# Optimization experiments

Hardware: AMD Instinct MI355X
Metric: run time of the kernel (lower is better)

The kernel has to match this reference:

```python
import jax, jax.numpy as jnp
import numpy as np

LN_EPS = 1e-5  # torch LayerNorm default
EPS = 1e-8     # slot-attention eps

def _ln(x, g, b):
    m = jnp.mean(x, axis=-1, keepdims=True)
    v = jnp.mean(jnp.square(x - m), axis=-1, keepdims=True)
    return (x - m) * jax.lax.rsqrt(v + LN_EPS) * g + b

def setup_inputs() -> dict:
    key = jax.random.key(0)
    ks = jax.random.split(key, 16)
    b, d, n_s, h = 131072, 256, 16, 256
    w_scale = d ** -0.5
    return {
        "inputs": jax.random.normal(ks[0], (b, 1, d), jnp.float32),
        "noise": jax.random.normal(ks[1], (n_s, d), jnp.float32),
        "slots_mu": jax.random.normal(ks[2], (1, d), jnp.float32),
        "slots_sigma": jax.random.uniform(ks[3], (1, d), jnp.float32),
        "Wq": jax.random.normal(ks[4], (d, d), jnp.float32) * w_scale,
        "bq": jnp.zeros((d,), jnp.float32),
        "Wk": jax.random.normal(ks[5], (d, d), jnp.float32) * w_scale,
        "bk": jnp.zeros((d,), jnp.float32),
        "Wv": jax.random.normal(ks[6], (d, d), jnp.float32) * w_scale,
        "bv": jnp.zeros((d,), jnp.float32),
        "W_ih": jax.random.normal(ks[7], (3 * d, d), jnp.float32) * w_scale,
        "W_hh": jax.random.normal(ks[8], (3 * d, d), jnp.float32) * w_scale,
        "b_ih": jnp.zeros((3 * d,), jnp.float32),
        "b_hh": jnp.zeros((3 * d,), jnp.float32),
        "W1": jax.random.normal(ks[9], (h, d), jnp.float32) * w_scale,
        "b1": jnp.zeros((h,), jnp.float32),
        "W2": jax.random.normal(ks[10], (d, h), jnp.float32) * (h ** -0.5),
        "b2": jnp.zeros((d,), jnp.float32),
        "g_in": jnp.ones((d,), jnp.float32),
        "be_in": jnp.zeros((d,), jnp.float32),
        "g_s": jnp.ones((d,), jnp.float32),
        "be_s": jnp.zeros((d,), jnp.float32),
        "g_f": jnp.ones((d,), jnp.float32),
        "be_f": jnp.zeros((d,), jnp.float32),
    }

def reference(inputs, noise, slots_mu, slots_sigma, Wq, bq, Wk, bk, Wv, bv,
              W_ih, W_hh, b_ih, b_hh, W1, b1, W2, b2,
              g_in, be_in, g_s, be_s, g_f, be_f):
    b, w, d = inputs.shape  # w == 1 required by the module's LayerNorm(dim)
    x = inputs.reshape(b, w * d)
    scale = d ** -0.5
    iters = 3

    slots = slots_mu + slots_sigma * noise  # (n_s, d), reparameterized normal

    x = _ln(x, g_in, be_in)
    k = x @ Wk.T + bk  # (b, d)
    v = x @ Wv.T + bv  # (b, d)

    for _ in range(iters):
        slots_prev = slots
        s = _ln(slots, g_s, be_s)
        q = s @ Wq.T + bq                      # (n_s, d)
        dots = jnp.einsum('nd,bd->nb', q, k) * scale
        attn = jax.nn.softmax(dots, axis=0) + EPS   # softmax over slots
        attn = attn / jnp.sum(attn, axis=-1, keepdims=True)
        updates = jnp.einsum('bd,nb->nd', v, attn)  # (n_s, d)
        # torch GRUCell
        gx = updates @ W_ih.T + b_ih                # (n_s, 3d)
        gh = slots_prev @ W_hh.T + b_hh
        xr, xz, xn = jnp.split(gx, 3, axis=-1)
        hr, hz, hn = jnp.split(gh, 3, axis=-1)
        r = jax.nn.sigmoid(xr + hr)
        z = jax.nn.sigmoid(xz + hz)
        n = jnp.tanh(xn + r * hn)
        slots = (1.0 - z) * n + z * slots_prev
        ff = jax.nn.relu(_ln(slots, g_f, be_f) @ W1.T + b1) @ W2.T + b2
        slots = slots + ff
    return slots
```

## Files before the change

### kernel.cpp

```cpp
#include <hip/hip_runtime.h>
#include <stdint.h>

#define B_ROWS 131072
#define SCALE 0.0625f
#define LN_EPS 1e-5f
#define ATTN_EPS 1e-8f

#define BIG_BLOCKS 512
#define BIG_THREADS 512
#define ROWS_PER_BLOCK (B_ROWS / BIG_BLOCKS)
#define ROWS_PER_WAVE  (ROWS_PER_BLOCK / 8)
#define NSLICE 64

#define WS_PARTU 0
#define WS_PARTS (WS_PARTU + 512*4096)
#define WS_U     (WS_PARTS + 512*16)
#define WS_S     (WS_U + 4096)
#define WS_SLOTS (WS_S + 64)
#define WS_MID   (WS_SLOTS + 4096)
#define WS_GX    (WS_MID + 4096)
#define WS_GH    (WS_GX + 12288)
#define WS_H1    (WS_GH + 12288)
#define WS_QKG   (WS_H1 + 4096)
#define WS_QB    (WS_QKG + 4096)
#define WS_WIHV  (WS_QB + 64)
#define WS_BGX   (WS_WIHV + 196608)
#define WS_WQKG  (WS_BGX + 768)
#define WS_U2G   (WS_WQKG + 65536)
#define WS_U1    (WS_U2G + 256)
#define WS_C1    (WS_U1 + 256)

__global__ __launch_bounds__(256) void k_pre1(
    const float* __restrict__ Wq, const float* __restrict__ bq,
    const float* __restrict__ Wk, const float* __restrict__ bk,
    const float* __restrict__ Wv, const float* __restrict__ bv,
    const float* __restrict__ W_ih, const float* __restrict__ b_ih,
    const float* __restrict__ g_in, const float* __restrict__ be_in,
    float* __restrict__ ws)
{
  int bid = blockIdx.x, t = threadIdx.x;
  int wave = t >> 6, lane = t & 63;
  if (bid < 256) {
#pragma unroll
    for (int q = 0; q < 4; q++)
      ws[WS_PARTU + bid * 1024 + q * 256 + t] = 0.f;
  } else {
#pragma unroll
    for (int q = 0; q < 4; q++)
      ws[WS_PARTS + q * 256 + t] = 0.f;
  }
  if (bid < 192) {
    __shared__ __align__(16) float sW[4 * 256];
    __shared__ __align__(16) float sBv[256];
    int j0 = bid * 4;
#pragma unroll
    for (int r = 0; r < 4; r++) sW[r * 256 + t] = W_ih[(j0 + r) * 256 + t];
    sBv[t] = bv[t];
    __syncthreads();
    int d = t;
    float a0 = 0.f, a1 = 0.f, a2 = 0.f, a3 = 0.f;
#pragma unroll 8
    for (int dd = 0; dd < 256; dd++) {
      float v = Wv[dd * 256 + d];
      a0 = fmaf(sW[0 * 256 + dd], v, a0);
      a1 = fmaf(sW[1 * 256 + dd], v, a1);
      a2 = fmaf(sW[2 * 256 + dd], v, a2);
      a3 = fmaf(sW[3 * 256 + dd], v, a3);
    }
    ws[WS_WIHV + (j0 + 0) * 256 + d] = a0;
    ws[WS_WIHV + (j0 + 1) * 256 + d] = a1;
    ws[WS_WIHV + (j0 + 2) * 256 + d] = a2;
    ws[WS_WIHV + (j0 + 3) * 256 + d] = a3;
    float s = 0.f;
#pragma unroll
    for (int q = 0; q < 4; q++) {
      int idx = lane * 4 + q;
      s = fmaf(sW[wave * 256 + idx], sBv[idx], s);
    }
#pragma unroll
    for (int m = 1; m <= 32; m <<= 1) s += __shfl_xor(s, m);
    if (lane == 0) ws[WS_BGX + j0 + wave] = b_ih[j0 + wave] + s;
  } else if (bid < 256) {
    __shared__ __align__(16) float sKc[4 * 256];
    __shared__ __align__(16) float sBq[256];
    int c0 = (bid - 192) * 4;
#pragma unroll
    for (int r = 0; r < 4; r++) sKc[r * 256 + t] = Wk[t * 256 + c0 + r];
    sBq[t] = bq[t];
    __syncthreads();
    int d = t;
    float a0 = 0.f, a1 = 0.f, a2 = 0.f, a3 = 0.f;
#pragma unroll 8
    for (int i = 0; i < 256; i++) {
      float wq = Wq[i * 256 + d];
      a0 = fmaf(wq, sKc[0 * 256 + i], a0);
      a1 = fmaf(wq, sKc[1 * 256 + i], a1);
      a2 = fmaf(wq, sKc[2 * 256 + i], a2);
      a3 = fmaf(wq, sKc[3 * 256 + i], a3);
    }
    ws[WS_WQKG + (c0 + 0) * 256 + d] = SCALE * g_in[c0 + 0] * a0;
    ws[WS_WQKG + (c0 + 1) * 256 + d] = SCALE * g_in[c0 + 1] * a1;
    ws[WS_WQKG + (c0 + 2) * 256 + d] = SCALE * g_in[c0 + 2] * a2;
    ws[WS_WQKG + (c0 + 3) * 256 + d] = SCALE * g_in[c0 + 3] * a3;
    float s = 0.f;
#pragma unroll
    for (int q = 0; q < 4; q++) {
      int idx = lane * 4 + q;
      s = fmaf(sBq[idx], sKc[wave * 256 + idx], s);
    }
#pragma unroll
    for (int m = 1; m <= 32; m <<= 1) s += __shfl_xor(s, m);
    if (lane == 0) ws[WS_U2G + c0 + wave] = SCALE * g_in[c0 + wave] * s;
  } else {
    __shared__ __align__(16) float sBe[256];
    __shared__ __align__(16) float sT2[256];
    sBe[t] = be_in[t];
    __syncthreads();
    float a = 0.f;
#pragma unroll 8
    for (int dp = 0; dp < 256; dp += 4) {
      float4 w = *(const float4*)(Wk + t * 256 + dp);
      a = fmaf(w.x, sBe[dp], fmaf(w.y, sBe[dp + 1],
          fmaf(w.z, sBe[dp + 2], fmaf(w.w, sBe[dp + 3], a))));
    }
    sT2[t] = a + bk[t];
    __syncthreads();
    float u = 0.f;
#pragma unroll 8
    for (int i = 0; i < 256; i++)
      u = fmaf(Wq[i * 256 + t], sT2[i], u);
    ws[WS_U1 + t] = u;
    if (wave == 0) {
      float s = 0.f;
#pragma unroll
      for (int q = 0; q < 4; q++) {
        int idx = lane * 4 + q;
        s = fmaf(bq[idx], sT2[idx], s);
      }
#pragma unroll
      for (int m = 1; m <= 32; m <<= 1) s += __shfl_xor(s, m);
      if (lane == 0) ws[WS_C1] = s;
    }
  }
}

__global__ __launch_bounds__(256) void k_qkg(
    const float* __restrict__ noise, const float* __restrict__ mu,
    const float* __restrict__ sigma, const float* __restrict__ g_s,
    const float* __restrict__ be_s, float* __restrict__ ws, int init)
{
  __shared__ __align__(16) float sS[16 * 260];
  __shared__ __align__(16) float sAux[512];
  __shared__ __align__(16) float sStat[32];
  int bid = blockIdx.x, t = threadIdx.x;
  for (int n = 0; n < 16; n++) {
    float v;
    if (init) v = fmaf(sigma[t], noise[n * 256 + t], mu[t]);
    else      v = ws[WS_SLOTS + n * 256 + t];
    sS[n * 260 + t] = v;
    if (init && bid == 0) ws[WS_SLOTS + n * 256 + t] = v;
  }
  __syncthreads();
  { int n = t >> 4, c = t & 15;
    float s1 = 0.f, s2 = 0.f;
    for (int k = 0; k < 16; k++) {
      float x = sS[n * 260 + c * 16 + k];
      s1 += x; s2 = fmaf(x, x, s2);
    }
    sAux[n * 16 + c] = s1; sAux[256 + n * 16 + c] = s2; }
  __syncthreads();
  if (t < 16) {
    float s1 = 0.f, s2 = 0.f;
    for (int c = 0; c < 16; c++) { s1 += sAux[t * 16 + c]; s2 += sAux[256 + t * 16 + c]; }
    float m = s1 * (1.f / 256.f);
    float v = fmaxf(fmaf(-m, m, s2 * (1.f / 256.f)), 0.f);
    sStat[t] = m; sStat[16 + t] = rsqrtf(v + LN_EPS);
  }
  __syncthreads();
  { float gs = g_s[t], bs = be_s[t];
    for (int n = 0; n < 16; n++) {
      float m = sStat[n], rs = sStat[16 + n];
      sS[n * 260 + t] = fmaf((sS[n * 260 + t] - m) * rs, gs, bs);
    } }
  __syncthreads();
  if (bid < 64) {
    int cr = t >> 6, n = (t >> 2) & 15, ks = t & 3;
    int c = bid * 4 + cr;
    const float* wrow = ws + WS_WQKG + c * 256 + ks * 64;
    const float* srow = &sS[n * 260 + ks * 64];
    float acc = 0.f;
#pragma unroll
    for (int i = 0; i < 16; i++) {
      float4 w = *(const float4*)(wrow + i * 4);
      float4 s4 = *(const float4*)(srow + i * 4);
      acc = fmaf(w.x, s4.x, fmaf(w.y, s4.y, fmaf(w.z, s4.z, fmaf(w.w, s4.w, acc))));
    }
    sAux[t] = acc;
    __syncthreads();
    if (t < 64) {
      int cr2 = t >> 4, n2 = t & 15;
      int c2 = bid * 4 + cr2;
      int b = cr2 * 64 + n2 * 4;
      float s = sAux[b] + sAux[b + 1] + sAux[b + 2] + sAux[b + 3];
      ws[WS_QKG + n2 * 256 + c2] = s + ws[WS_U2G + c2];
    }
  } else {
    int n = t >> 4, ks = t & 15;
    float acc = 0.f;
    for (int k = 0; k < 16; k++)
      acc = fmaf(sS[n * 260 + ks * 16 + k], ws[WS_U1 + ks * 16 + k], acc);
    sAux[t] = acc;
    __syncthreads();
    if (t < 16) {
      float s = 0.f;
      for (int k = 0; k < 16; k++) s += sAux[t * 16 + k];
      ws[WS_QB + t] = SCALE * (s + ws[WS_C1]);
    }
  }
}

__global__ __launch_bounds__(512, 2) void k_big(
    const float* __restrict__ X, float* __restrict__ ws)
{
  __shared__ __align__(16) float red[4 * 4096];
  __shared__ __align__(16) float redS[128];
  int t = threadIdx.x;
  int wave = t >> 6, lane = t & 63;
  int p = lane >> 4, g = lane & 15;

  const float* qkg = ws + WS_QKG;
  float qw[4][16];
  float qs[4];
#pragma unroll
  for (int i = 0; i < 4; i++) {
    const float* rp = qkg + (4 * p + i) * 256 + g * 16;
#pragma unroll
    for (int jq = 0; jq < 4; jq++) {
      float4 v4 = *(const float4*)(rp + 4 * jq);
      qw[i][4 * jq + 0] = v4.x; qw[i][4 * jq + 1] = v4.y;
      qw[i][4 * jq + 2] = v4.z; qw[i][4 * jq + 3] = v4.w;
    }
    float s = 0.f;
#pragma unroll
    for (int j = 0; j < 16; j++) s += qw[i][j];
    qs[i] = s;
  }
#pragma unroll
  for (int m = 1; m <= 8; m <<= 1) {
#pragma unroll
    for (int i = 0; i < 4; i++) qs[i] += __shfl_xor(qs[i], m);
  }
  float qb0[4];
  {
    float4 q4 = *(const float4*)(ws + WS_QB + 4 * p);
    qb0[0] = q4.x; qb0[1] = q4.y; qb0[2] = q4.z; qb0[3] = q4.w;
  }

  float P[4][16];
#pragma unroll
  for (int i = 0; i < 4; i++)
#pragma unroll
    for (int j = 0; j < 16; j++) P[i][j] = 0.f;
  float Q[4] = {0.f, 0.f, 0.f, 0.f};
  float Sa[4] = {0.f, 0.f, 0.f, 0.f};

  size_t rowbase = (size_t)blockIdx.x * ROWS_PER_BLOCK + (size_t)wave * ROWS_PER_WAVE;
  const float* base = X + rowbase * 256 + g * 16;

  float4 cA0 = *(const float4*)(base + 0);
  float4 cB0 = *(const float4*)(base + 4);
  float4 cC0 = *(const float4*)(base + 8);
  float4 cD0 = *(const float4*)(base + 12);
  float4 cA1 = *(const float4*)(base + 256);
  float4 cB1 = *(const float4*)(base + 260);
  float4 cC1 = *(const float4*)(base + 264);
  float4 cD1 = *(const float4*)(base + 268);

#pragma unroll 1
  for (int r = 0; r < ROWS_PER_WAVE; r += 2) {
    const float* nx = base + (size_t)((r + 2 < ROWS_PER_WAVE) ? (r + 2) : 0) * 256;
    float4 pA0 = *(const float4*)(nx + 0);
    float4 pB0 = *(const float4*)(nx + 4);
    float4 pC0 = *(const float4*)(nx + 8);
    float4 pD0 = *(const float4*)(nx + 12);
    float4 pA1 = *(const float4*)(nx + 256);
    float4 pB1 = *(const float4*)(nx + 260);
    float4 pC1 = *(const float4*)(nx + 264);
    float4 pD1 = *(const float4*)(nx + 268);

    float x0[16], x1[16];
    x0[0] = cA0.x; x0[1] = cA0.y; x0[2] = cA0.z; x0[3] = cA0.w;
    x0[4] = cB0.x; x0[5] = cB0.y; x0[6] = cB0.z; x0[7] = cB0.w;
    x0[8] = cC0.x; x0[9] = cC0.y; x0[10] = cC0.z; x0[11] = cC0.w;
    x0[12] = cD0.x; x0[13] = cD0.y; x0[14] = cD0.z; x0[15] = cD0.w;
    x1[0] = cA1.x; x1[1] = cA1.y; x1[2] = cA1.z; x1[3] = cA1.w;
    x1[4] = cB1.x; x1[5] = cB1.y; x1[6] = cB1.z; x1[7] = cB1.w;
    x1[8] = cC1.x; x1[9] = cC1.y; x1[10] = cC1.z; x1[11] = cC1.w;
    x1[12] = cD1.x; x1[13] = cD1.y; x1[14] = cD1.z; x1[15] = cD1.w;

    float s10 = 0.f, s20 = 0.f, s11 = 0.f, s21 = 0.f;
    float d0[4] = {0.f, 0.f, 0.f, 0.f};
    float d1[4] = {0.f, 0.f, 0.f, 0.f};
#pragma unroll
    for (int j = 0; j < 16; j++) {
      s10 += x0[j]; s20 = fmaf(x0[j], x0[j], s20);
      s11 += x1[j]; s21 = fmaf(x1[j], x1[j], s21);
#pragma unroll
      for (int i = 0; i < 4; i++) {
        d0[i] = fmaf(qw[i][j], x0[j], d0[i]);
        d1[i] = fmaf(qw[i][j], x1[j], d1[i]);
      }
    }
#pragma unroll
    for (int m = 1; m <= 8; m <<= 1) {
      s10 += __shfl_xor(s10, m); s11 += __shfl_xor(s11, m);
      s20 += __shfl_xor(s20, m); s21 += __shfl_xor(s21, m);
#pragma unroll
      for (int i = 0; i < 4; i++) {
        d0[i] += __shfl_xor(d0[i], m);
        d1[i] += __shfl_xor(d1[i], m);
      }
    }
    float mean0 = s10 * (1.f / 256.f), mean1 = s11 * (1.f / 256.f);
    float var0 = fmaxf(fmaf(-mean0, mean0, s20 * (1.f / 256.f)), 0.f);
    float var1 = fmaxf(fmaf(-mean1, mean1, s21 * (1.f / 256.f)), 0.f);
    float rs0 = rsqrtf(var0 + LN_EPS), rs1 = rsqrtf(var1 + LN_EPS);
    float mrs0 = mean0 * rs0, mrs1 = mean1 * rs1;

    float dsc0[4], dsc1[4];
#pragma unroll
    for (int i = 0; i < 4; i++) {
      dsc0[i] = fmaf(rs0, d0[i], fmaf(-mrs0, qs[i], qb0[i]));
      dsc1[i] = fmaf(rs1, d1[i], fmaf(-mrs1, qs[i], qb0[i]));
    }

    float mx0 = fmaxf(fmaxf(dsc0[0], dsc0[1]), fmaxf(dsc0[2], dsc0[3]));
    float mx1 = fmaxf(fmaxf(dsc1[0], dsc1[1]), fmaxf(dsc1[2], dsc1[3]));
    mx0 = fmaxf(mx0, __shfl_xor(mx0, 16)); mx1 = fmaxf(mx1, __shfl_xor(mx1, 16));
    mx0 = fmaxf(mx0, __shfl_xor(mx0, 32)); mx1 = fmaxf(mx1, __shfl_xor(mx1, 32));
    float e0[4], e1[4];
#pragma unroll
    for (int i = 0; i < 4; i++) {
      e0[i] = __expf(dsc0[i] - mx0);
      e1[i] = __expf(dsc1[i] - mx1);
    }
    float se0 = e0[0] + e0[1] + e0[2] + e0[3];
    float se1 = e1[0] + e1[1] + e1[2] + e1[3];
    se0 += __shfl_xor(se0, 16); se1 += __shfl_xor(se1, 16);
    se0 += __shfl_xor(se0, 32); se1 += __shfl_xor(se1, 32);
    float inv0 = 1.0f / se0, inv1 = 1.0f / se1;
    float a0v[4], ar0[4], a1v[4], ar1[4];
#pragma unroll
    for (int i = 0; i < 4; i++) {
      a0v[i] = fmaf(e0[i], inv0, ATTN_EPS); ar0[i] = a0v[i] * rs0;
      a1v[i] = fmaf(e1[i], inv1, ATTN_EPS); ar1[i] = a1v[i] * rs1;
    }

#pragma unroll
    for (int j = 0; j < 16; j++) {
#pragma unroll
      for (int i = 0; i < 4; i++) {
        P[i][j] = fmaf(ar0[i], x0[j], P[i][j]);
        P[i][j] = fmaf(ar1[i], x1[j], P[i][j]);
      }
    }
#pragma unroll
    for (int i = 0; i < 4; i++) {
      Q[i] = fmaf(a0v[i], mrs0, Q[i]);
      Q[i] = fmaf(a1v[i], mrs1, Q[i]);
      Sa[i] += a0v[i];
      Sa[i] += a1v[i];
    }

    cA0 = pA0; cB0 = pB0; cC0 = pC0; cD0 = pD0;
    cA1 = pA1; cB1 = pB1; cC1 = pC1; cD1 = pD1;
  }

  int slot = wave & 3;
  if (wave < 4) {
#pragma unroll
    for (int i = 0; i < 4; i++) {
#pragma unroll
      for (int jq = 0; jq < 4; jq++) {
        float4 v4;
        v4.x = P[i][4 * jq + 0] - Q[i]; v4.y = P[i][4 * jq + 1] - Q[i];
        v4.z = P[i][4 * jq + 2] - Q[i]; v4.w = P[i][4 * jq + 3] - Q[i];
        *(float4*)&red[slot * 4096 + (4 * p + i) * 256 + g * 16 + jq * 4] = v4;
      }
    }
  }
  if (g == 0) {
#pragma unroll
    for (int i = 0; i < 4; i++) redS[wave * 16 + 4 * p + i] = Sa[i];
  }
  __syncthreads();
  if (wave >= 4) {
#pragma unroll
    for (int i = 0; i < 4; i++) {
#pragma unroll
      for (int jq = 0; jq < 4; jq++) {
        float4* dst = (float4*)&red[slot * 4096 + (4 * p + i) * 256 + g * 16 + jq * 4];
        float4 c = *dst;
        c.x += P[i][4 * jq + 0] - Q[i]; c.y += P[i][4 * jq + 1] - Q[i];
        c.z += P[i][4 * jq + 2] - Q[i]; c.w += P[i][4 * jq + 3] - Q[i];
        *dst = c;
      }
    }
  }
  __syncthreads();
  int slice = blockIdx.x & 63;
#pragma unroll
  for (int k = 0; k < 8; k++) {
    int idx = k * 512 + t;
    float v = red[idx] + red[4096 + idx] + red[8192 + idx] + red[12288 + idx];
    atomicAdd(&ws[WS_PARTU + (size_t)slice * 4096 + idx], v);
  }
  if (t < 16) {
    float sv = 0.f;
#pragma unroll
    for (int w = 0; w < 8; w++) sv += redS[w * 16 + t];
    atomicAdd(&ws[WS_PARTS + slice * 16 + t], sv);
  }
}

__global__ __launch_bounds__(256) void k_red(float* __restrict__ ws)
{
  __shared__ __align__(16) float sAux[256];
  int bid = blockIdx.x, t = threadIdx.x;
  if (bid < 256) {
    int el = t & 15, wg = t >> 4;
    int e = bid * 16 + el;
    float acc = 0.f;
#pragma unroll
    for (int k = 0; k < 4; k++) {
      size_t idx = WS_PARTU + (size_t)(wg + k * 16) * 4096 + e;
      acc += ws[idx];
      ws[idx] = 0.f;
    }
    sAux[t] = acc;
    __syncthreads();
    if (t < 16) {
      float s = 0.f;
      for (int w = 0; w < 16; w++) s += sAux[w * 16 + t];
      ws[WS_U + bid * 16 + t] = s;
    }
  } else {
    int n = t & 15, wg = t >> 4;
    float acc = 0.f;
#pragma unroll
    for (int k = 0; k < 4; k++) {
      int idx = WS_PARTS + (wg + k * 16) * 16 + n;
      acc += ws[idx];
      ws[idx] = 0.f;
    }
    sAux[t] = acc;
    __syncthreads();
    if (t < 16) {
      float s = 0.f;
      for (int w = 0; w < 16; w++) s += sAux[w * 16 + t];
      ws[WS_S + t] = s;
    }
  }
}

__global__ __launch_bounds__(256) void k_gxgh(
    const float* __restrict__ W_hh, const float* __restrict__ b_hh,
    const float* __restrict__ g_in, const float* __restrict__ be_in,
    float* __restrict__ ws)
{
  __shared__ __align__(16) float sU[16 * 260];
  __shared__ __align__(16) float sInv[16];
  int bid = blockIdx.x, t = threadIdx.x;
  bool isgx = bid < 64;
  if (isgx && t < 16) sInv[t] = 1.0f / ws[WS_S + t];
  __syncthreads();
  if (isgx) {
    float gi = g_in[t], bi = be_in[t];
    for (int n = 0; n < 16; n++)
      sU[n * 260 + t] = fmaf(gi * ws[WS_U + n * 256 + t], sInv[n], bi);
  } else {
    for (int n = 0; n < 16; n++)
      sU[n * 260 + t] = ws[WS_SLOTS + n * 256 + t];
  }
  __syncthreads();
  int jr = t >> 4, n = t & 15;
  if (jr < 12) {
    int j = (isgx ? bid : bid - 64) * 12 + jr;
    const float* srow = &sU[n * 260];
    const float* wrow = isgx ? (ws + WS_WIHV + j * 256) : (W_hh + j * 256);
    float acc = isgx ? ws[WS_BGX + j] : b_hh[j];
#pragma unroll 8
    for (int k = 0; k < 64; k++) {
      float4 w = *(const float4*)(wrow + k * 4);
      float4 s4 = *(const float4*)(srow + k * 4);
      acc = fmaf(w.x, s4.x, fmaf(w.y, s4.y, fmaf(w.z, s4.z, fmaf(w.w, s4.w, acc))));
    }
    if (isgx) ws[WS_GX + n * 768 + j] = acc;
    else      ws[WS_GH + n * 768 + j] = acc;
  }
}

__global__ __launch_bounds__(256) void k_midh1(
    const float* __restrict__ W1, const float* __restrict__ b1,
    const float* __restrict__ g_f, const float* __restrict__ be_f,
    float* __restrict__ ws)
{
  __shared__ __align__(16) float sM[16 * 260];
  __shared__ __align__(16) float sAux[512];
  __shared__ __align__(16) float sStat[32];
  int bid = blockIdx.x, t = threadIdx.x;
  for (int n = 0; n < 16; n++) {
    float xr = ws[WS_GX + n * 768 + t],       hr = ws[WS_GH + n * 768 + t];
    float xz = ws[WS_GX + n * 768 + 256 + t], hz = ws[WS_GH + n * 768 + 256 + t];
    float xn = ws[WS_GX + n * 768 + 512 + t], hn = ws[WS_GH + n * 768 + 512 + t];
    float sp = ws[WS_SLOTS + n * 256 + t];
    float r = 1.f / (1.f + __expf(-(xr + hr)));
    float z = 1.f / (1.f + __expf(-(xz + hz)));
    float nn = tanhf(fmaf(r, hn, xn));
    float mid = fmaf(z, sp - nn, nn);
    sM[n * 260 + t] = mid;
    if (bid == 0) ws[WS_MID + n * 256 + t] = mid;
  }
  __syncthreads();
  { int n = t >> 4, c = t & 15;
    float s1 = 0.f, s2 = 0.f;
    for (int k = 0; k < 16; k++) {
      float x = sM[n * 260 + c * 16 + k];
      s1 += x; s2 = fmaf(x, x, s2);
    }
    sAux[n * 16 + c] = s1; sAux[256 + n * 16 + c] = s2; }
  __syncthreads();
  if (t < 16) {
    float s1 = 0.f, s2 = 0.f;
    for (int c = 0; c < 16; c++) { s1 += sAux[t * 16 + c]; s2 += sAux[256 + t * 16 + c]; }
    float m = s1 * (1.f / 256.f);
    float v = fmaxf(fmaf(-m, m, s2 * (1.f / 256.f)), 0.f);
    sStat[t] = m; sStat[16 + t] = rsqrtf(v + LN_EPS);
  }
  __syncthreads();
  { float gf = g_f[t], bf = be_f[t];
    for (int n = 0; n < 16; n++) {
      float m = sStat[n], rs = sStat[16 + n];
      sM[n * 260 + t] = fmaf((sM[n * 260 + t] - m) * rs, gf, bf);
    } }
  __syncthreads();
  int jr = t >> 6, n = (t >> 2) & 15, ks = t & 3;
  int j = bid * 4 + jr;
  const float* wrow = W1 + j * 256 + ks * 64;
  const float* srow = &sM[n * 260 + ks * 64];
  float acc = 0.f;
#pragma unroll
  for (int k = 0; k < 16; k++) {
    float4 w = *(const float4*)(wrow + k * 4);
    float4 s4 = *(const float4*)(srow + k * 4);
    acc = fmaf(w.x, s4.x, fmaf(w.y, s4.y, fmaf(w.z, s4.z, fmaf(w.w, s4.w, acc))));
  }
  sAux[t] = acc;
  __syncthreads();
  if (t < 64) {
    int jr2 = t >> 4, n2 = t & 15;
    int j2 = bid * 4 + jr2;
    int b = jr2 * 64 + n2 * 4;
    float s = sAux[b] + sAux[b + 1] + sAux[b + 2] + sAux[b + 3] + b1[j2];
    ws[WS_H1 + n2 * 256 + j2] = fmaxf(s, 0.f);
  }
}

__global__ __launch_bounds__(256) void k_ffnew(
    const float* __restrict__ W2, const float* __restrict__ b2v,
    float* __restrict__ out, float* __restrict__ ws)
{
  __shared__ __align__(16) float sH[16 * 260];
  __shared__ __align__(16) float sAux[256];
  int bid = blockIdx.x, t = threadIdx.x;
  for (int n = 0; n < 16; n++)
    sH[n * 260 + t] = ws[WS_H1 + n * 256 + t];
  __syncthreads();
  int dr = t >> 6, n = (t >> 2) & 15, ks = t & 3;
  int d = bid * 4 + dr;
  const float* wrow = W2 + d * 256 + ks * 64;
  const float* srow = &sH[n * 260 + ks * 64];
  float acc = 0.f;
#pragma unroll
  for (int k = 0; k < 16; k++) {
    float4 w = *(const float4*)(wrow + k * 4);
    float4 s4 = *(const float4*)(srow + k * 4);
    acc = fmaf(w.x, s4.x, fmaf(w.y, s4.y, fmaf(w.z, s4.z, fmaf(w.w, s4.w, acc))));
  }
  sAux[t] = acc;
  __syncthreads();
  if (t < 64) {
    int dr2 = t >> 4, n2 = t & 15;
    int d2 = bid * 4 + dr2;
    int b = dr2 * 64 + n2 * 4;
    float s = sAux[b] + sAux[b + 1] + sAux[b + 2] + sAux[b + 3]
            + b2v[d2] + ws[WS_MID + n2 * 256 + d2];
    ws[WS_SLOTS + n2 * 256 + d2] = s;
    out[n2 * 256 + d2] = s;
  }
}

extern "C" void kernel_launch(void* const* d_in, const int* in_sizes, int n_in,
                              void* d_out, int out_size, void* d_ws, size_t ws_size,
                              hipStream_t stream)
{
  (void)in_sizes; (void)n_in; (void)out_size; (void)ws_size;
  const float* inputs = (const float*)d_in[0];
  const float* noise  = (const float*)d_in[1];
  const float* mu     = (const float*)d_in[2];
  const float* sigma  = (const float*)d_in[3];
  const float* Wq     = (const float*)d_in[4];
  const float* bq     = (const float*)d_in[5];
  const float* Wk     = (const float*)d_in[6];
  const float* bk     = (const float*)d_in[7];
  const float* Wv     = (const float*)d_in[8];
  const float* bv     = (const float*)d_in[9];
  const float* W_ih   = (const float*)d_in[10];
  const float* W_hh   = (const float*)d_in[11];
  const float* b_ih   = (const float*)d_in[12];
  const float* b_hh   = (const float*)d_in[13];
  const float* W1     = (const float*)d_in[14];
  const float* b1     = (const float*)d_in[15];
  const float* W2     = (const float*)d_in[16];
  const float* b2     = (const float*)d_in[17];
  const float* g_in   = (const float*)d_in[18];
  const float* be_in  = (const float*)d_in[19];
  const float* g_s    = (const float*)d_in[20];
  const float* be_s   = (const float*)d_in[21];
  const float* g_f    = (const float*)d_in[22];
  const float* be_f   = (const float*)d_in[23];
  float* ws = (float*)d_ws;
  float* out = (float*)d_out;

  hipLaunchKernelGGL(k_pre1, dim3(257), dim3(256), 0, stream,
                     Wq, bq, Wk, bk, Wv, bv, W_ih, b_ih, g_in, be_in, ws);
  hipLaunchKernelGGL(k_qkg, dim3(65), dim3(256), 0, stream,
                     noise, mu, sigma, g_s, be_s, ws, 1);
  for (int it = 0; it < 3; it++) {
    hipLaunchKernelGGL(k_big, dim3(BIG_BLOCKS), dim3(BIG_THREADS), 0, stream, inputs, ws);
    hipLaunchKernelGGL(k_red, dim3(257), dim3(256), 0, stream, ws);
    hipLaunchKernelGGL(k_gxgh, dim3(128), dim3(256), 0, stream,
                       W_hh, b_hh, g_in, be_in, ws);
    hipLaunchKernelGGL(k_midh1, dim3(64), dim3(256), 0, stream,
                       W1, b1, g_f, be_f, ws);
    hipLaunchKernelGGL(k_ffnew, dim3(64), dim3(256), 0, stream,
                       W2, b2, out, ws);
    if (it < 2)
      hipLaunchKernelGGL(k_qkg, dim3(65), dim3(256), 0, stream,
                         noise, mu, sigma, g_s, be_s, ws, 0);
  }
}
```

Measured before the change: 557.5 us.

## Cache per-row LayerNorm stats, shrink atomic slices, fold reduction into gxgh

```diff
diff --git a/kernel.cpp b/kernel.cpp
--- a/kernel.cpp
+++ b/kernel.cpp
@@ -10,9 +10,11 @@
 #define BIG_THREADS 512
 #define ROWS_PER_BLOCK (B_ROWS / BIG_BLOCKS)
 #define ROWS_PER_WAVE  (ROWS_PER_BLOCK / 8)
-#define NSLICE 64
+#define NSLICE 8
 
 #define WS_PARTU 0
+#define WS_RS    (WS_PARTU + 64*4096)
+#define WS_MRS   (WS_RS + B_ROWS)
 #define WS_PARTS (WS_PARTU + 512*4096)
 #define WS_U     (WS_PARTS + 512*16)
 #define WS_S     (WS_U + 4096)
@@ -40,14 +42,12 @@
 {
   int bid = blockIdx.x, t = threadIdx.x;
   int wave = t >> 6, lane = t & 63;
-  if (bid < 256) {
+  if (bid < 32) {
 #pragma unroll
     for (int q = 0; q < 4; q++)
       ws[WS_PARTU + bid * 1024 + q * 256 + t] = 0.f;
-  } else {
-#pragma unroll
-    for (int q = 0; q < 4; q++)
-      ws[WS_PARTS + q * 256 + t] = 0.f;
+  } else if (bid == 256) {
+    if (t < 128) ws[WS_PARTS + t] = 0.f;
   }
   if (bid < 192) {
     __shared__ __align__(16) float sW[4 * 256];
@@ -220,7 +220,7 @@
 }
 
 __global__ __launch_bounds__(512, 2) void k_big(
-    const float* __restrict__ X, float* __restrict__ ws)
+    const float* __restrict__ X, float* __restrict__ ws, int it)
 {
   __shared__ __align__(16) float red[4 * 4096];
   __shared__ __align__(16) float redS[128];
@@ -288,6 +288,13 @@
     float4 pC1 = *(const float4*)(nx + 264);
     float4 pD1 = *(const float4*)(nx + 268);
 
+    size_t row = rowbase + r;
+    float rsL0 = 0.f, mrsL0 = 0.f, rsL1 = 0.f, mrsL1 = 0.f;
+    if (it != 0) {
+      rsL0 = ws[WS_RS + row];      mrsL0 = ws[WS_MRS + row];
+      rsL1 = ws[WS_RS + row + 1];  mrsL1 = ws[WS_MRS + row + 1];
+    }
+
     float x0[16], x1[16];
     x0[0] = cA0.x; x0[1] = cA0.y; x0[2] = cA0.z; x0[3] = cA0.w;
     x0[4] = cB0.x; x0[5] = cB0.y; x0[6] = cB0.z; x0[7] = cB0.w;
@@ -301,31 +308,60 @@
     float s10 = 0.f, s20 = 0.f, s11 = 0.f, s21 = 0.f;
     float d0[4] = {0.f, 0.f, 0.f, 0.f};
     float d1[4] = {0.f, 0.f, 0.f, 0.f};
-#pragma unroll
-    for (int j = 0; j < 16; j++) {
-      s10 += x0[j]; s20 = fmaf(x0[j], x0[j], s20);
-      s11 += x1[j]; s21 = fmaf(x1[j], x1[j], s21);
-#pragma unroll
-      for (int i = 0; i < 4; i++) {
-        d0[i] = fmaf(qw[i][j], x0[j], d0[i]);
-        d1[i] = fmaf(qw[i][j], x1[j], d1[i]);
-      }
-    }
-#pragma unroll
-    for (int m = 1; m <= 8; m <<= 1) {
-      s10 += __shfl_xor(s10, m); s11 += __shfl_xor(s11, m);
-      s20 += __shfl_xor(s20, m); s21 += __shfl_xor(s21, m);
-#pragma unroll
-      for (int i = 0; i < 4; i++) {
-        d0[i] += __shfl_xor(d0[i], m);
-        d1[i] += __shfl_xor(d1[i], m);
-      }
-    }
-    float mean0 = s10 * (1.f / 256.f), mean1 = s11 * (1.f / 256.f);
-    float var0 = fmaxf(fmaf(-mean0, mean0, s20 * (1.f / 256.f)), 0.f);
-    float var1 = fmaxf(fmaf(-mean1, mean1, s21 * (1.f / 256.f)), 0.f);
-    float rs0 = rsqrtf(var0 + LN_EPS), rs1 = rsqrtf(var1 + LN_EPS);
-    float mrs0 = mean0 * rs0, mrs1 = mean1 * rs1;
+    if (it == 0) {
+#pragma unroll
+      for (int j = 0; j < 16; j++) {
+        s10 += x0[j]; s20 = fmaf(x0[j], x0[j], s20);
+        s11 += x1[j]; s21 = fmaf(x1[j], x1[j], s21);
+#pragma unroll
+        for (int i = 0; i < 4; i++) {
+          d0[i] = fmaf(qw[i][j], x0[j], d0[i]);
+          d1[i] = fmaf(qw[i][j], x1[j], d1[i]);
+        }
+      }
+#pragma unroll
+      for (int m = 1; m <= 8; m <<= 1) {
+        s10 += __shfl_xor(s10, m); s11 += __shfl_xor(s11, m);
+        s20 += __shfl_xor(s20, m); s21 += __shfl_xor(s21, m);
+#pragma unroll
+        for (int i = 0; i < 4; i++) {
+          d0[i] += __shfl_xor(d0[i], m);
+          d1[i] += __shfl_xor(d1[i], m);
+        }
+      }
+    } else {
+#pragma unroll
+      for (int j = 0; j < 16; j++) {
+#pragma unroll
+        for (int i = 0; i < 4; i++) {
+          d0[i] = fmaf(qw[i][j], x0[j], d0[i]);
+          d1[i] = fmaf(qw[i][j], x1[j], d1[i]);
+        }
+      }
+#pragma unroll
+      for (int m = 1; m <= 8; m <<= 1) {
+#pragma unroll
+        for (int i = 0; i < 4; i++) {
+          d0[i] += __shfl_xor(d0[i], m);
+          d1[i] += __shfl_xor(d1[i], m);
+        }
+      }
+    }
+
+    float rs0, rs1, mrs0, mrs1;
+    if (it == 0) {
+      float mean0 = s10 * (1.f / 256.f), mean1 = s11 * (1.f / 256.f);
+      float var0 = fmaxf(fmaf(-mean0, mean0, s20 * (1.f / 256.f)), 0.f);
+      float var1 = fmaxf(fmaf(-mean1, mean1, s21 * (1.f / 256.f)), 0.f);
+      rs0 = rsqrtf(var0 + LN_EPS); rs1 = rsqrtf(var1 + LN_EPS);
+      mrs0 = mean0 * rs0; mrs1 = mean1 * rs1;
+      if (lane == 0) {
+        ws[WS_RS + row] = rs0;      ws[WS_MRS + row] = mrs0;
+        ws[WS_RS + row + 1] = rs1;  ws[WS_MRS + row + 1] = mrs1;
+      }
+    } else {
+      rs0 = rsL0; mrs0 = mrsL0; rs1 = rsL1; mrs1 = mrsL1;
+    }
 
     float dsc0[4], dsc1[4];
 #pragma unroll
@@ -408,7 +444,7 @@
     }
   }
   __syncthreads();
-  int slice = blockIdx.x & 63;
+  int slice = blockIdx.x & 7;
 #pragma unroll
   for (int k = 0; k < 8; k++) {
     int idx = k * 512 + t;
@@ -420,46 +456,6 @@
 #pragma unroll
     for (int w = 0; w < 8; w++) sv += redS[w * 16 + t];
     atomicAdd(&ws[WS_PARTS + slice * 16 + t], sv);
-  }
-}
-
-__global__ __launch_bounds__(256) void k_red(float* __restrict__ ws)
-{
-  __shared__ __align__(16) float sAux[256];
-  int bid = blockIdx.x, t = threadIdx.x;
-  if (bid < 256) {
-    int el = t & 15, wg = t >> 4;
-    int e = bid * 16 + el;
-    float acc = 0.f;
-#pragma unroll
-    for (int k = 0; k < 4; k++) {
-      size_t idx = WS_PARTU + (size_t)(wg + k * 16) * 4096 + e;
-      acc += ws[idx];
-      ws[idx] = 0.f;
-    }
-    sAux[t] = acc;
-    __syncthreads();
-    if (t < 16) {
-      float s = 0.f;
-      for (int w = 0; w < 16; w++) s += sAux[w * 16 + t];
-      ws[WS_U + bid * 16 + t] = s;
-    }
-  } else {
-    int n = t & 15, wg = t >> 4;
-    float acc = 0.f;
-#pragma unroll
-    for (int k = 0; k < 4; k++) {
-      int idx = WS_PARTS + (wg + k * 16) * 16 + n;
-      acc += ws[idx];
-      ws[idx] = 0.f;
-    }
-    sAux[t] = acc;
-    __syncthreads();
-    if (t < 16) {
-      float s = 0.f;
-      for (int w = 0; w < 16; w++) s += sAux[w * 16 + t];
-      ws[WS_S + t] = s;
-    }
   }
 }
 
@@ -472,12 +468,22 @@
   __shared__ __align__(16) float sInv[16];
   int bid = blockIdx.x, t = threadIdx.x;
   bool isgx = bid < 64;
-  if (isgx && t < 16) sInv[t] = 1.0f / ws[WS_S + t];
+  if (isgx && t < 16) {
+    float s = 0.f;
+#pragma unroll
+    for (int sl = 0; sl < NSLICE; sl++) s += ws[WS_PARTS + sl * 16 + t];
+    sInv[t] = 1.0f / s;
+  }
   __syncthreads();
   if (isgx) {
     float gi = g_in[t], bi = be_in[t];
-    for (int n = 0; n < 16; n++)
-      sU[n * 260 + t] = fmaf(gi * ws[WS_U + n * 256 + t], sInv[n], bi);
+    for (int n = 0; n < 16; n++) {
+      float acc = 0.f;
+#pragma unroll
+      for (int sl = 0; sl < NSLICE; sl++)
+        acc += ws[WS_PARTU + (size_t)sl * 4096 + n * 256 + t];
+      sU[n * 260 + t] = fmaf(gi * acc, sInv[n], bi);
+    }
   } else {
     for (int n = 0; n < 16; n++)
       sU[n * 260 + t] = ws[WS_SLOTS + n * 256 + t];
@@ -509,6 +515,12 @@
   __shared__ __align__(16) float sAux[512];
   __shared__ __align__(16) float sStat[32];
   int bid = blockIdx.x, t = threadIdx.x;
+  {
+    int gid = bid * 256 + t;
+    ws[WS_PARTU + gid] = 0.f;
+    ws[WS_PARTU + 16384 + gid] = 0.f;
+    if (gid < 128) ws[WS_PARTS + gid] = 0.f;
+  }
   for (int n = 0; n < 16; n++) {
     float xr = ws[WS_GX + n * 768 + t],       hr = ws[WS_GH + n * 768 + t];
     float xz = ws[WS_GX + n * 768 + 256 + t], hz = ws[WS_GH + n * 768 + 256 + t];
@@ -637,8 +649,8 @@
   hipLaunchKernelGGL(k_qkg, dim3(65), dim3(256), 0, stream,
                      noise, mu, sigma, g_s, be_s, ws, 1);
   for (int it = 0; it < 3; it++) {
-    hipLaunchKernelGGL(k_big, dim3(BIG_BLOCKS), dim3(BIG_THREADS), 0, stream, inputs, ws);
-    hipLaunchKernelGGL(k_red, dim3(257), dim3(256), 0, stream, ws);
+    hipLaunchKernelGGL(k_big, dim3(BIG_BLOCKS), dim3(BIG_THREADS), 0, stream,
+                       inputs, ws, it);
     hipLaunchKernelGGL(k_gxgh, dim3(128), dim3(256), 0, stream,
                        W_hh, b_hh, g_in, be_in, ws);
     hipLaunchKernelGGL(k_midh1, dim3(64), dim3(256), 0, stream,
```

Result: no change. 553.1 us (-0.8%).
